# Performance work log

Measured on AMD Instinct MI355X. Metric: run time of the kernel, lower is better.

## Reference

```python
import jax, jax.numpy as jnp
import numpy as np

DELTA = 16
KAPPA = 4
ACTION_LOSS_WEIGHT = 0.2
ACTION_CLASS_WEIGHT = 10.0
NEG = -1e30  # sentinel for masked-out positions

B, T = 1024, 4096


def setup_inputs() -> dict:
    key = jax.random.key(0)
    k1, k2, k3, k4 = jax.random.split(key, 4)
    s1s2_log_probs = jax.random.normal(k1, (B, T, 2), dtype=jnp.float32)
    action_log_probs = jax.random.normal(k2, (B, T, 1), dtype=jnp.float32)
    lens = jax.random.randint(k3, (B,), T // 2, T + 1, dtype=jnp.int32)
    video_level_scores = jax.random.uniform(k4, (B,), dtype=jnp.float32)
    return {
        "s1s2_log_probs": s1s2_log_probs,
        "action_log_probs": action_log_probs,
        "lens": lens,
        "video_level_scores": video_level_scores,
    }


def _optimal_state_change(s1s2_probs, action_probs, lens):
    """Per-video optimal (state1, action, state2) alignment with delta spacing.

    Maximizes p1[s1] * pa[ac] * p2[s2] s.t. s1 <= ac - DELTA, ac + DELTA <= s2 < len,
    via prefix/suffix cumulative maxima (O(T) DP per video, fully vectorized).
    Returns integer targets: state_targets in {0,1,2}, action_targets in {0,1,2}.
    """
    Bn, Tn, _ = s1s2_probs.shape
    p1, p2 = s1s2_probs[..., 0], s1s2_probs[..., 1]
    pa = action_probs[..., 0]
    t = jnp.arange(Tn)
    valid = t[None, :] < lens[:, None]  # [B,T]
    p1m = jnp.where(valid, p1, NEG)
    p2m = jnp.where(valid, p2, NEG)
    pre = jax.lax.cummax(p1m, axis=1)                                  # max p1[0..t]
    suf = jnp.flip(jax.lax.cummax(jnp.flip(p2m, 1), axis=1), 1)        # max p2[t..T-1]
    pad = jnp.full((Bn, DELTA), NEG, dtype=p1.dtype)
    pre_s = jnp.concatenate([pad, pre[:, : Tn - DELTA]], axis=1)       # best s1 <= ac-DELTA
    suf_s = jnp.concatenate([suf[:, DELTA:], pad], axis=1)             # best s2 >= ac+DELTA
    ok = (pre_s > NEG / 2) & (suf_s > NEG / 2) & valid
    score = jnp.where(ok, pre_s * pa * suf_s, NEG)
    ac = jnp.argmax(score, axis=1)                                     # [B]
    s1 = jnp.argmax(jnp.where(t[None, :] <= (ac - DELTA)[:, None], p1m, NEG), axis=1)
    s2 = jnp.argmax(jnp.where(t[None, :] >= (ac + DELTA)[:, None], p2m, NEG), axis=1)
    state_t = ((t[None, :] == s1[:, None]).astype(jnp.int32)
               + 2 * (t[None, :] == s2[:, None]).astype(jnp.int32))
    dist = jnp.abs(t[None, :] - ac[:, None])
    action_t = jnp.where(valid, jnp.where(dist <= KAPPA, 2, 1), 0)
    return state_t, action_t


def reference(s1s2_log_probs, action_log_probs, lens, video_level_scores):
    s1s2_probs = jax.nn.softmax(s1s2_log_probs, axis=-1)
    action_probs = jax.nn.sigmoid(action_log_probs)
    state_t, action_t = _optimal_state_change(
        jax.lax.stop_gradient(s1s2_probs), jax.lax.stop_gradient(action_probs), lens)

    # state loss: CE over 2 classes, masked where target == 0 (ignore)
    logp = jax.nn.log_softmax(s1s2_log_probs, axis=-1)          # [B,T,2]
    cls = jnp.clip(state_t - 1, 0, None)
    state_loss = -jnp.take_along_axis(logp, cls[..., None], axis=-1)[..., 0]
    state_loss = state_loss * (state_t != 0).astype(logp.dtype)

    # action loss: weighted BCE-with-logits
    z = action_log_probs[..., 0]                                 # [B,T]
    y = (action_t == 2).astype(z.dtype)
    bce = jnp.maximum(z, 0.0) - z * y + jnp.log1p(jnp.exp(-jnp.abs(z)))
    w = (action_t == 1).astype(z.dtype) + ACTION_CLASS_WEIGHT * (action_t == 2).astype(z.dtype)
    action_loss = bce * w

    state_loss = state_loss * video_level_scores[:, None]
    action_loss = action_loss * video_level_scores[:, None]
    return jnp.sum(state_loss), ACTION_LOSS_WEIGHT * jnp.sum(action_loss)
```

## Files before the change

### kernel.cpp

```cpp
#include <hip/hip_runtime.h>
#include <math.h>


#define T_LEN 4096
#define NTH   512
#define CH    8
#define PADS  9
#define DELTA 16
#define NEGV  (-1e30f)
#define NEGH  (-5e29f)

__device__ __forceinline__ float frcp(float x) { return __builtin_amdgcn_rcpf(x); }

__device__ __forceinline__ void amax_comb(float& v, int& i, float ov, int oi) {
  if (ov > v || (ov == v && oi < i)) { v = ov; i = oi; }
}

__global__ __launch_bounds__(512, 4) void lftc_main(
    const float* __restrict__ s1s2,
    const float* __restrict__ act,
    const int*   __restrict__ lens,
    const float* __restrict__ vls,
    float* __restrict__ ws)
{
  __shared__ float P1s[NTH * PADS];
  __shared__ float cm1[NTH];
  __shared__ float cm2[NTH];
  __shared__ float wag1[8], wag2[8];
  __shared__ float redv[8];  __shared__ int redi[8];
  __shared__ float redv2[8]; __shared__ int redi2[8];
  __shared__ float redv3[8]; __shared__ int redi3[8];

  const int b    = blockIdx.x;
  const int tid  = threadIdx.x;
  const int lane = tid & 63;
  const int wv   = tid >> 6;
  const int len  = lens[b];
  const float w  = vls[b];

  const float* __restrict__ srow = s1s2 + (size_t)b * T_LEN * 2;
  const float* __restrict__ zrow = act  + (size_t)b * T_LEN;

  const int j    = tid;
  const int base = j * CH;

  float4 sv[4];
  {
    const float4* sp4 = reinterpret_cast<const float4*>(srow + 2 * base);
#pragma unroll
    for (int k = 0; k < 4; k++) sv[k] = sp4[k];
  }
  float4 zv[2];
  {
    const float4* zp4 = reinterpret_cast<const float4*>(zrow + base);
    zv[0] = zp4[0]; zv[1] = zp4[1];
  }
  const float* sf = reinterpret_cast<const float*>(sv);
  const float* z  = reinterpret_cast<const float*>(zv);

  float p1r[CH];
  float m1 = NEGV, m2 = NEGV, sp_part = 0.f;
#pragma unroll
  for (int i = 0; i < CH; i++) {
    float lx = sf[2 * i], ly = sf[2 * i + 1];
    float p  = frcp(1.f + __expf(ly - lx));
    bool  v  = (base + i) < len;
    float p1m = v ? p : NEGV;
    float p2m = v ? 1.f - p : NEGV;
    p1r[i] = p1m;
    P1s[j * PADS + i] = p1m;
    m1 = fmaxf(m1, p1m);
    m2 = fmaxf(m2, p2m);
    float zi = z[i];
    if (v) sp_part += fmaxf(zi, 0.f) + __logf(1.f + __expf(-fabsf(zi)));
  }

  {
    float pm = m1;
#pragma unroll
    for (int off = 1; off < 64; off <<= 1) {
      float o = __shfl_up(pm, off);
      if (lane >= off) pm = fmaxf(pm, o);
    }
    float sm = m2;
#pragma unroll
    for (int off = 1; off < 64; off <<= 1) {
      float o = __shfl_down(sm, off);
      if (lane + off < 64) sm = fmaxf(sm, o);
    }
    if (lane == 63) wag1[wv] = pm;
    if (lane == 0)  wag2[wv] = sm;
    __syncthreads();
    float addp = NEGV, adds = NEGV;
#pragma unroll
    for (int q = 0; q < 8; q++) {
      if (q < wv) addp = fmaxf(addp, wag1[q]);
      if (q > wv) adds = fmaxf(adds, wag2[q]);
    }
    cm1[tid] = fmaxf(pm, addp);
    cm2[tid] = fmaxf(sm, adds);
    __syncthreads();
  }

  float best = NEGV;
  int   bidx = base;
  {
    float rs[CH];
    if (j <= NTH - 3) {
      float run = (j + 3 <= NTH - 1) ? cm2[j + 3] : NEGV;
      const int b2 = (j + 2) * PADS;
#pragma unroll
      for (int i = CH - 1; i >= 0; --i) {
        float p1n = P1s[b2 + i];
        float p2n = (p1n > NEGH) ? 1.f - p1n : NEGV;
        run = fmaxf(run, p2n);
        rs[i] = run;
      }
    }
    float prerun = (j >= 3) ? cm1[j - 3] : NEGV;
    const int b1 = (j - 2) * PADS;
#pragma unroll
    for (int i = 0; i < CH; i++) {
      float pre_s = NEGV;
      if (j >= 2) { prerun = fmaxf(prerun, P1s[b1 + i]); pre_s = prerun; }
      float suf_s = (j <= NTH - 3) ? rs[i] : NEGV;
      int t = base + i;
      if (pre_s > NEGH && suf_s > NEGH && t < len) {
        float pa = frcp(1.f + __expf(-z[i]));
        float sc = (pre_s * pa) * suf_s;
        if (sc > best) { best = sc; bidx = t; }
      }
    }
  }
#pragma unroll
  for (int off = 32; off; off >>= 1) {
    float ov = __shfl_down(best, off);
    int   oi = __shfl_down(bidx, off);
    amax_comb(best, bidx, ov, oi);
  }
  if (lane == 0) { redv[wv] = best; redi[wv] = bidx; }
  __syncthreads();
  int ac;
  {
    float v = redv[0]; int i = redi[0];
#pragma unroll
    for (int q = 1; q < 8; q++) amax_comb(v, i, redv[q], redi[q]);
    ac = i;
  }

  {
    float v1 = NEGV; int i1 = 0;
    float v2 = NEGV; int i2 = 0;
    const int e1   = ac - DELTA;
    const int s2lo = ac + DELTA;
#pragma unroll
    for (int k = 0; k < CH; k++) {
      int t = base + k;
      float p1v = p1r[k];
      if (t <= e1 && p1v > v1) { v1 = p1v; i1 = t; }
      float p2v = (p1v > NEGH) ? 1.f - p1v : NEGV;
      if (t >= s2lo && p2v > v2) { v2 = p2v; i2 = t; }
    }
#pragma unroll
    for (int off = 32; off; off >>= 1) {
      float ov1 = __shfl_down(v1, off); int oi1 = __shfl_down(i1, off);
      amax_comb(v1, i1, ov1, oi1);
      float ov2 = __shfl_down(v2, off); int oi2 = __shfl_down(i2, off);
      amax_comb(v2, i2, ov2, oi2);
    }
    if (lane == 0) { redv2[wv] = v1; redi2[wv] = i1; redv3[wv] = v2; redi3[wv] = i2; }
  }

#pragma unroll
  for (int k = 0; k < CH; k++) {
    int t = base + k;
    int d = t - ac;
    if (d >= -4 && d <= 4 && t < len) {
      float zi = z[k];
      float b0 = fmaxf(zi, 0.f) + __logf(1.f + __expf(-fabsf(zi)));
      sp_part += 10.f * (b0 - zi) - b0;
    }
  }
  float s = sp_part;
#pragma unroll
  for (int off = 32; off; off >>= 1) s += __shfl_down(s, off);
  if (lane == 0) wag1[wv] = s;
  __syncthreads();
  if (tid == 0) {
    float tot = 0.f;
#pragma unroll
    for (int q = 0; q < 8; q++) tot += wag1[q];

    float sv1 = redv2[0]; int s1 = redi2[0];
    float sv2 = redv3[0]; int s2 = redi3[0];
    for (int q = 1; q < 8; q++) {
      amax_comb(sv1, s1, redv2[q], redi2[q]);
      amax_comb(sv2, s2, redv3[q], redi3[q]);
    }
    float a0 = srow[2 * (size_t)s1], a1 = srow[2 * (size_t)s1 + 1];
    float c0 = srow[2 * (size_t)s2], c1 = srow[2 * (size_t)s2 + 1];
    float d1 = a1 - a0;
    float loss1 = fmaxf(d1, 0.f) + __logf(1.f + __expf(-fabsf(d1)));
    float d2 = c0 - c1;
    float loss2 = fmaxf(d2, 0.f) + __logf(1.f + __expf(-fabsf(d2)));

    ws[2 * (size_t)b]     = w * (loss1 + loss2);
    ws[2 * (size_t)b + 1] = 0.2f * w * tot;
  }
}

__global__ void lftc_reduce(const float* __restrict__ ws, float* __restrict__ out, int B) {
  __shared__ float a0[4], a1[4];
  const int tid  = threadIdx.x;
  const int lane = tid & 63;
  const int wv   = tid >> 6;
  float s0 = 0.f, s1 = 0.f;
  for (int i = tid; i < B; i += 256) {
    s0 += ws[2 * (size_t)i];
    s1 += ws[2 * (size_t)i + 1];
  }
#pragma unroll
  for (int off = 32; off; off >>= 1) {
    s0 += __shfl_down(s0, off);
    s1 += __shfl_down(s1, off);
  }
  if (lane == 0) { a0[wv] = s0; a1[wv] = s1; }
  __syncthreads();
  if (tid == 0) {
    out[0] = a0[0] + a0[1] + a0[2] + a0[3];
    out[1] = a1[0] + a1[1] + a1[2] + a1[3];
  }
}

extern "C" void kernel_launch(void* const* d_in, const int* in_sizes, int n_in,
                              void* d_out, int out_size, void* d_ws, size_t ws_size,
                              hipStream_t stream) {
  const float* s1s2 = (const float*)d_in[0];
  const float* act  = (const float*)d_in[1];
  const int*   lens = (const int*)d_in[2];
  const float* vls  = (const float*)d_in[3];
  float* out = (float*)d_out;
  float* ws  = (float*)d_ws;

  const int B = in_sizes[2];

  lftc_main<<<B, NTH, 0, stream>>>(s1s2, act, lens, vls, ws);
  lftc_reduce<<<1, 256, 0, stream>>>(ws, out, B);
}
```

Before: 99.14 us.

## Use 1024 threads per video with 4 elements each, merge softplus passes

Each block now uses 1024 threads, each handling 4 time steps instead of 8, with 16 wavefronts. The shared-memory neighbour offsets for the delta window are adjusted to match. The softplus accumulation is moved into a single pass after the argmax instead of being split across two passes. Minor vectorized float2 loads are used in the final gather and in the reduce kernel. More threads give more latency hiding, but the scan and argmax reductions now combine more wavefronts per block.

```diff
diff --git a/kernel.cpp b/kernel.cpp
--- a/kernel.cpp
+++ b/kernel.cpp
@@ -3,9 +3,11 @@
 
 
 #define T_LEN 4096
-#define NTH   512
-#define CH    8
-#define PADS  9
+#define NTH   1024
+#define NW    16
+#define CH    4
+#define PADS  5
+#define DCH   4
 #define DELTA 16
 #define NEGV  (-1e30f)
 #define NEGH  (-5e29f)
@@ -16,7 +18,7 @@
   if (ov > v || (ov == v && oi < i)) { v = ov; i = oi; }
 }
 
-__global__ __launch_bounds__(512, 4) void lftc_main(
+__global__ __launch_bounds__(NTH, 8) void lftc_main(
     const float* __restrict__ s1s2,
     const float* __restrict__ act,
     const int*   __restrict__ lens,
@@ -26,17 +28,16 @@
   __shared__ float P1s[NTH * PADS];
   __shared__ float cm1[NTH];
   __shared__ float cm2[NTH];
-  __shared__ float wag1[8], wag2[8];
-  __shared__ float redv[8];  __shared__ int redi[8];
-  __shared__ float redv2[8]; __shared__ int redi2[8];
-  __shared__ float redv3[8]; __shared__ int redi3[8];
+  __shared__ float wag1[NW], wag2[NW];
+  __shared__ float redv[NW];  __shared__ int redi[NW];
+  __shared__ float redv2[NW]; __shared__ int redi2[NW];
+  __shared__ float redv3[NW]; __shared__ int redi3[NW];
 
   const int b    = blockIdx.x;
   const int tid  = threadIdx.x;
   const int lane = tid & 63;
   const int wv   = tid >> 6;
   const int len  = lens[b];
-  const float w  = vls[b];
 
   const float* __restrict__ srow = s1s2 + (size_t)b * T_LEN * 2;
   const float* __restrict__ zrow = act  + (size_t)b * T_LEN;
@@ -44,35 +45,28 @@
   const int j    = tid;
   const int base = j * CH;
 
-  float4 sv[4];
+  float4 sv0, sv1, zv;
   {
     const float4* sp4 = reinterpret_cast<const float4*>(srow + 2 * base);
-#pragma unroll
-    for (int k = 0; k < 4; k++) sv[k] = sp4[k];
-  }
-  float4 zv[2];
-  {
-    const float4* zp4 = reinterpret_cast<const float4*>(zrow + base);
-    zv[0] = zp4[0]; zv[1] = zp4[1];
-  }
-  const float* sf = reinterpret_cast<const float*>(sv);
-  const float* z  = reinterpret_cast<const float*>(zv);
+    sv0 = sp4[0]; sv1 = sp4[1];
+    zv  = *reinterpret_cast<const float4*>(zrow + base);
+  }
+  float z[CH]   = {zv.x, zv.y, zv.z, zv.w};
+  float lx[CH]  = {sv0.x, sv0.z, sv1.x, sv1.z};
+  float ly[CH]  = {sv0.y, sv0.w, sv1.y, sv1.w};
 
   float p1r[CH];
-  float m1 = NEGV, m2 = NEGV, sp_part = 0.f;
+  float m1 = NEGV, m2 = NEGV;
 #pragma unroll
   for (int i = 0; i < CH; i++) {
-    float lx = sf[2 * i], ly = sf[2 * i + 1];
-    float p  = frcp(1.f + __expf(ly - lx));
-    bool  v  = (base + i) < len;
+    float p   = frcp(1.f + __expf(ly[i] - lx[i]));
+    bool  v   = (base + i) < len;
     float p1m = v ? p : NEGV;
     float p2m = v ? 1.f - p : NEGV;
     p1r[i] = p1m;
     P1s[j * PADS + i] = p1m;
     m1 = fmaxf(m1, p1m);
     m2 = fmaxf(m2, p2m);
-    float zi = z[i];
-    if (v) sp_part += fmaxf(zi, 0.f) + __logf(1.f + __expf(-fabsf(zi)));
   }
 
   {
@@ -93,7 +87,7 @@
     __syncthreads();
     float addp = NEGV, adds = NEGV;
 #pragma unroll
-    for (int q = 0; q < 8; q++) {
+    for (int q = 0; q < NW; q++) {
       if (q < wv) addp = fmaxf(addp, wag1[q]);
       if (q > wv) adds = fmaxf(adds, wag2[q]);
     }
@@ -106,9 +100,9 @@
   int   bidx = base;
   {
     float rs[CH];
-    if (j <= NTH - 3) {
-      float run = (j + 3 <= NTH - 1) ? cm2[j + 3] : NEGV;
-      const int b2 = (j + 2) * PADS;
+    if (j <= NTH - 1 - DCH) {
+      float run = (j + DCH + 1 <= NTH - 1) ? cm2[j + DCH + 1] : NEGV;
+      const int b2 = (j + DCH) * PADS;
 #pragma unroll
       for (int i = CH - 1; i >= 0; --i) {
         float p1n = P1s[b2 + i];
@@ -117,13 +111,13 @@
         rs[i] = run;
       }
     }
-    float prerun = (j >= 3) ? cm1[j - 3] : NEGV;
-    const int b1 = (j - 2) * PADS;
+    float prerun = (j >= DCH + 1) ? cm1[j - DCH - 1] : NEGV;
+    const int b1 = (j - DCH) * PADS;
 #pragma unroll
     for (int i = 0; i < CH; i++) {
       float pre_s = NEGV;
-      if (j >= 2) { prerun = fmaxf(prerun, P1s[b1 + i]); pre_s = prerun; }
-      float suf_s = (j <= NTH - 3) ? rs[i] : NEGV;
+      if (j >= DCH) { prerun = fmaxf(prerun, P1s[b1 + i]); pre_s = prerun; }
+      float suf_s = (j <= NTH - 1 - DCH) ? rs[i] : NEGV;
       int t = base + i;
       if (pre_s > NEGH && suf_s > NEGH && t < len) {
         float pa = frcp(1.f + __expf(-z[i]));
@@ -144,7 +138,7 @@
   {
     float v = redv[0]; int i = redi[0];
 #pragma unroll
-    for (int q = 1; q < 8; q++) amax_comb(v, i, redv[q], redi[q]);
+    for (int q = 1; q < NW; q++) amax_comb(v, i, redv[q], redi[q]);
     ac = i;
   }
 
@@ -171,14 +165,15 @@
     if (lane == 0) { redv2[wv] = v1; redi2[wv] = i1; redv3[wv] = v2; redi3[wv] = i2; }
   }
 
+  float sp_part = 0.f;
 #pragma unroll
   for (int k = 0; k < CH; k++) {
     int t = base + k;
-    int d = t - ac;
-    if (d >= -4 && d <= 4 && t < len) {
+    if (t < len) {
       float zi = z[k];
       float b0 = fmaxf(zi, 0.f) + __logf(1.f + __expf(-fabsf(zi)));
-      sp_part += 10.f * (b0 - zi) - b0;
+      int d = t - ac;
+      sp_part += (d >= -4 && d <= 4) ? 10.f * (b0 - zi) : b0;
     }
   }
   float s = sp_part;
@@ -189,21 +184,22 @@
   if (tid == 0) {
     float tot = 0.f;
 #pragma unroll
-    for (int q = 0; q < 8; q++) tot += wag1[q];
-
-    float sv1 = redv2[0]; int s1 = redi2[0];
-    float sv2 = redv3[0]; int s2 = redi3[0];
-    for (int q = 1; q < 8; q++) {
-      amax_comb(sv1, s1, redv2[q], redi2[q]);
-      amax_comb(sv2, s2, redv3[q], redi3[q]);
-    }
-    float a0 = srow[2 * (size_t)s1], a1 = srow[2 * (size_t)s1 + 1];
-    float c0 = srow[2 * (size_t)s2], c1 = srow[2 * (size_t)s2 + 1];
-    float d1 = a1 - a0;
+    for (int q = 0; q < NW; q++) tot += wag1[q];
+
+    float sv_1 = redv2[0]; int s1 = redi2[0];
+    float sv_2 = redv3[0]; int s2 = redi3[0];
+    for (int q = 1; q < NW; q++) {
+      amax_comb(sv_1, s1, redv2[q], redi2[q]);
+      amax_comb(sv_2, s2, redv3[q], redi3[q]);
+    }
+    float2 q1 = *reinterpret_cast<const float2*>(srow + 2 * (size_t)s1);
+    float2 q2 = *reinterpret_cast<const float2*>(srow + 2 * (size_t)s2);
+    float d1 = q1.y - q1.x;
     float loss1 = fmaxf(d1, 0.f) + __logf(1.f + __expf(-fabsf(d1)));
-    float d2 = c0 - c1;
+    float d2 = q2.x - q2.y;
     float loss2 = fmaxf(d2, 0.f) + __logf(1.f + __expf(-fabsf(d2)));
 
+    float w = vls[b];
     ws[2 * (size_t)b]     = w * (loss1 + loss2);
     ws[2 * (size_t)b + 1] = 0.2f * w * tot;
   }
@@ -215,9 +211,11 @@
   const int lane = tid & 63;
   const int wv   = tid >> 6;
   float s0 = 0.f, s1 = 0.f;
+  const float2* w2 = reinterpret_cast<const float2*>(ws);
   for (int i = tid; i < B; i += 256) {
-    s0 += ws[2 * (size_t)i];
-    s1 += ws[2 * (size_t)i + 1];
+    float2 p = w2[i];
+    s0 += p.x;
+    s1 += p.y;
   }
 #pragma unroll
   for (int off = 32; off; off >>= 1) {
```

Measured after the change: 108.6 us. 1.1x slower.
